# Performance work log

Measured on AMD Instinct MI355X. Metric: run time of the kernel, lower is better.

Reference implementation:

```python
import jax, jax.numpy as jnp
import numpy as np

B, S, D, H = 4, 2048, 1024, 16
HD = D // H  # head dim = 64


def setup_inputs() -> dict:
    key = jax.random.key(0)
    ks = jax.random.split(key, 11)
    sc = 1.0 / np.sqrt(D)
    return {
        "q": jax.random.normal(ks[0], (B, S, D), jnp.float32),
        "k": jax.random.normal(ks[1], (B, S, D), jnp.float32),
        "v": jax.random.normal(ks[2], (B, S, D), jnp.float32),
        "w_q": jax.random.normal(ks[3], (D, D), jnp.float32) * sc,
        "b_q": jnp.zeros((D,), jnp.float32),
        "w_k": jax.random.normal(ks[4], (D, D), jnp.float32) * sc,
        "b_k": jnp.zeros((D,), jnp.float32),
        "w_v": jax.random.normal(ks[5], (D, D), jnp.float32) * sc,
        "b_v": jnp.zeros((D,), jnp.float32),
        "w_fc": jax.random.normal(ks[6], (D, D), jnp.float32) * sc,
        "b_fc": jnp.zeros((D,), jnp.float32),
    }


def reference(q, k, v, w_q, b_q, w_k, b_k, w_v, b_v, w_fc, b_fc):
    scale = jnp.asarray(np.sqrt(HD), q.dtype)
    # QKV projections: [B,S,D] @ [D,D]^T (torch Linear: x @ W^T + b)
    Q = (q @ w_q.T + b_q).reshape(B, S, H, HD).transpose(0, 2, 1, 3)  # [B,H,S,HD]
    K = (k @ w_k.T + b_k).reshape(B, S, H, HD).transpose(0, 2, 1, 3)
    V = (v @ w_v.T + b_v).reshape(B, S, H, HD).transpose(0, 2, 1, 3)
    energy = jnp.einsum('bhqd,bhkd->bhqk', Q, K) / scale  # [B,H,S,S]
    attn = jax.nn.softmax(energy, axis=-1)  # dropout is identity in eval / p=0
    x = jnp.einsum('bhqk,bhkd->bhqd', attn, V)  # [B,H,S,HD]
    x = x.transpose(0, 2, 1, 3).reshape(B, S, D)
    return x @ w_fc.T + b_fc
```

## Files before the change

kernel.cpp:

```cpp
#include <hip/hip_runtime.h>
#include <stdint.h>

#define BN 4
#define SEQ 2048
#define DM 1024
#define NH 16
#define HD 64
#define ROWS (BN*SEQ)

typedef float  f32x4  __attribute__((ext_vector_type(4)));
typedef __bf16 bf16x8 __attribute__((ext_vector_type(8)));
typedef __bf16 bf16x4 __attribute__((ext_vector_type(4)));

#define QSCALE 0.18033688f

__device__ inline bf16x8 cvt8(const float* __restrict__ src) {
    float4 x0 = *(const float4*)src;
    float4 x1 = *(const float4*)(src + 4);
    bf16x8 r;
    r[0] = (__bf16)x0.x; r[1] = (__bf16)x0.y; r[2] = (__bf16)x0.z; r[3] = (__bf16)x0.w;
    r[4] = (__bf16)x1.x; r[5] = (__bf16)x1.y; r[6] = (__bf16)x1.z; r[7] = (__bf16)x1.w;
    return r;
}

__device__ inline void gl_lds16(const void* g, void* l) {
    __builtin_amdgcn_global_load_lds((const __attribute__((address_space(1))) uint32_t*)g,
                                     (__attribute__((address_space(3))) uint32_t*)l, 16, 0, 0);
}

__global__ __launch_bounds__(256) void cast3(
    const float* __restrict__ a0, const float* __restrict__ a1, const float* __restrict__ a2,
    __bf16* __restrict__ o0, __bf16* __restrict__ o1, __bf16* __restrict__ o2, int n8) {
    int t = blockIdx.x * 256 + threadIdx.x;
    if (t >= n8) return;
    const float* in = (blockIdx.y == 0) ? a0 : (blockIdx.y == 1) ? a1 : a2;
    __bf16* out     = (blockIdx.y == 0) ? o0 : (blockIdx.y == 1) ? o1 : o2;
    *(bf16x8*)&out[(size_t)t * 8] = cvt8(&in[(size_t)t * 8]);
}

__global__ __launch_bounds__(256) void cast4(
    const float* __restrict__ a0, const float* __restrict__ a1,
    const float* __restrict__ a2, const float* __restrict__ a3,
    __bf16* __restrict__ o0, __bf16* __restrict__ o1,
    __bf16* __restrict__ o2, __bf16* __restrict__ o3, int n8) {
    int t = blockIdx.x * 256 + threadIdx.x;
    if (t >= n8) return;
    const float* in = (blockIdx.y == 0) ? a0 : (blockIdx.y == 1) ? a1 : (blockIdx.y == 2) ? a2 : a3;
    __bf16* out     = (blockIdx.y == 0) ? o0 : (blockIdx.y == 1) ? o1 : (blockIdx.y == 2) ? o2 : o3;
    *(bf16x8*)&out[(size_t)t * 8] = cvt8(&in[(size_t)t * 8]);
}

#define GEMM_CORE_GLDS(Xp, Wp)                                                     \
    __shared__ __align__(16) __bf16 As[128 * 32];                                  \
    __shared__ __align__(16) __bf16 Bs[128 * 32];                                  \
    const int tid  = threadIdx.x;                                                  \
    const int lane = tid & 63;                                                     \
    const int wave = tid >> 6;                                                     \
    const int wm = (wave >> 1) * 64;                                               \
    const int wn = (wave & 1) * 64;                                                \
    const int c16 = lane & 15;                                                     \
    const int g8  = (lane >> 4) * 8;                                               \
    const int row0 = blockIdx.x * 128;                                             \
    const int col0 = blockIdx.y * 128;                                             \
    f32x4 acc[4][4] = {};                                                          \
    for (int k0 = 0; k0 < DM; k0 += 32) {                                          \
        __syncthreads();                                                           \
        _Pragma("unroll")                                                          \
        for (int h = 0; h < 2; h++) {                                              \
            int cidx = h * 256 + tid;                                              \
            gl_lds16(&Xp[(size_t)(row0 + (cidx >> 2)) * DM + k0 + (cidx & 3) * 8], \
                     &As[(size_t)(h * 256 + wave * 64) * 8]);                      \
            gl_lds16(&Wp[(size_t)(col0 + (cidx >> 2)) * DM + k0 + (cidx & 3) * 8], \
                     &Bs[(size_t)(h * 256 + wave * 64) * 8]);                      \
        }                                                                          \
        __syncthreads();                                                           \
        bf16x8 a[4], bfr[4];                                                       \
        _Pragma("unroll")                                                          \
        for (int i = 0; i < 4; i++) a[i]   = *(const bf16x8*)&As[(wm + i * 16 + c16) * 32 + g8]; \
        _Pragma("unroll")                                                          \
        for (int i = 0; i < 4; i++) bfr[i] = *(const bf16x8*)&Bs[(wn + i * 16 + c16) * 32 + g8]; \
        _Pragma("unroll")                                                          \
        for (int mi = 0; mi < 4; mi++)                                             \
            _Pragma("unroll")                                                      \
            for (int ni = 0; ni < 4; ni++)                                         \
                acc[mi][ni] = __builtin_amdgcn_mfma_f32_16x16x32_bf16(a[mi], bfr[ni], acc[mi][ni], 0, 0, 0); \
    }

__global__ __launch_bounds__(256) void gemm_qkv_f(
    const __bf16* __restrict__ qb, const __bf16* __restrict__ kb,
    const __bf16* __restrict__ vb,
    const __bf16* __restrict__ wqb, const __bf16* __restrict__ wkb,
    const __bf16* __restrict__ wvb,
    const float* __restrict__ bq, const float* __restrict__ bk,
    const float* __restrict__ bv,
    __bf16* __restrict__ Qp, __bf16* __restrict__ Kp, __bf16* __restrict__ Vt)
{
    const int z = blockIdx.z;
    const __bf16* X = (z == 0) ? qb : (z == 1) ? kb : vb;
    const __bf16* W = (z == 0) ? wqb : (z == 1) ? wkb : wvb;
    const float* bias = (z == 0) ? bq : (z == 1) ? bk : bv;

    GEMM_CORE_GLDS(X, W)

    if (z < 2) {
        __bf16* O = z ? Kp : Qp;
        const float qsc = z ? 1.0f : QSCALE;
        #pragma unroll
        for (int mi = 0; mi < 4; mi++) {
            int r0 = row0 + wm + mi * 16 + (lane >> 4) * 4;
            #pragma unroll
            for (int ni = 0; ni < 4; ni++) {
                int col = col0 + wn + ni * 16 + c16;
                float bsv = bias[col];
                int h = col >> 6, d = col & 63;
                #pragma unroll
                for (int i = 0; i < 4; i++) {
                    int r = r0 + i; int b = r >> 11, s = r & 2047;
                    O[((size_t)(b * NH + h) * SEQ + s) * HD + d] = (__bf16)((acc[mi][ni][i] + bsv) * qsc);
                }
            }
        }
    } else {
        #pragma unroll
        for (int mi = 0; mi < 4; mi++) {
            int r0 = row0 + wm + mi * 16 + (lane >> 4) * 4;
            #pragma unroll
            for (int ni = 0; ni < 4; ni++) {
                int col = col0 + wn + ni * 16 + c16;
                float bsv = bias[col];
                int h = col >> 6, d = col & 63;
                int b = r0 >> 11, s0 = r0 & 2047;
                size_t base = ((size_t)((b * NH + h) * HD + d)) * SEQ + s0;
                #pragma unroll
                for (int i = 0; i < 4; i++)
                    Vt[base + i] = (__bf16)(acc[mi][ni][i] + bsv);
            }
        }
    }
}

__global__ __launch_bounds__(256) void gemm_fc_f(
    const __bf16* __restrict__ Xc, const __bf16* __restrict__ Wfb,
    const float* __restrict__ bias, float* __restrict__ out)
{
    __shared__ __align__(16) __bf16 As[128 * 32];
    __shared__ __align__(16) __bf16 Bs[64 * 32];

    const int tid  = threadIdx.x;
    const int lane = tid & 63;
    const int wave = tid >> 6;
    const int wm = (wave >> 1) * 64;
    const int wn = (wave & 1) * 32;
    const int c16 = lane & 15;
    const int g8  = (lane >> 4) * 8;
    const int row0 = blockIdx.x * 128;
    const int col0 = blockIdx.y * 64;

    f32x4 acc[4][2] = {};
    for (int k0 = 0; k0 < DM; k0 += 32) {
        __syncthreads();
        #pragma unroll
        for (int h = 0; h < 2; h++) {
            int cidx = h * 256 + tid;
            gl_lds16(&Xc[(size_t)(row0 + (cidx >> 2)) * DM + k0 + (cidx & 3) * 8],
                     &As[(size_t)(h * 256 + wave * 64) * 8]);
        }
        gl_lds16(&Wfb[(size_t)(col0 + (tid >> 2)) * DM + k0 + (tid & 3) * 8],
                 &Bs[(size_t)(wave * 64) * 8]);
        __syncthreads();

        bf16x8 a[4], bfr[2];
        #pragma unroll
        for (int i = 0; i < 4; i++) a[i]   = *(const bf16x8*)&As[(wm + i * 16 + c16) * 32 + g8];
        #pragma unroll
        for (int i = 0; i < 2; i++) bfr[i] = *(const bf16x8*)&Bs[(wn + i * 16 + c16) * 32 + g8];
        #pragma unroll
        for (int mi = 0; mi < 4; mi++)
            #pragma unroll
            for (int ni = 0; ni < 2; ni++)
                acc[mi][ni] = __builtin_amdgcn_mfma_f32_16x16x32_bf16(a[mi], bfr[ni], acc[mi][ni], 0, 0, 0);
    }

    #pragma unroll
    for (int mi = 0; mi < 4; mi++) {
        int r0 = row0 + wm + mi * 16 + (lane >> 4) * 4;
        #pragma unroll
        for (int ni = 0; ni < 2; ni++) {
            int col = col0 + wn + ni * 16 + c16;
            float bsv = bias[col];
            #pragma unroll
            for (int i = 0; i < 4; i++)
                out[(size_t)(r0 + i) * DM + col] = acc[mi][ni][i] + bsv;
        }
    }
}

__global__ __launch_bounds__(256) void gemm_qk(
    const __bf16* __restrict__ qb, const __bf16* __restrict__ kb,
    const float* __restrict__ wqf, const float* __restrict__ wkf,
    const float* __restrict__ bq, const float* __restrict__ bk,
    __bf16* __restrict__ Qp, __bf16* __restrict__ Kp)
{
    const int z = blockIdx.z;
    const __bf16* X = z ? kb : qb;
    const float* W  = z ? wkf : wqf;
    const float* bias = z ? bk : bq;
    __bf16* O = z ? Kp : Qp;
    const float qsc = z ? 1.0f : QSCALE;

    __shared__ __align__(16) __bf16 As[128 * 32];
    __shared__ __align__(16) __bf16 Bs[128 * 32];

    const int tid  = threadIdx.x;
    const int lane = tid & 63;
    const int wave = tid >> 6;
    const int wm = (wave >> 1) * 64;
    const int wn = (wave & 1) * 64;
    const int c16 = lane & 15;
    const int g8  = (lane >> 4) * 8;
    const int row0 = blockIdx.x * 128;
    const int col0 = blockIdx.y * 128;
    const int brow = tid >> 1;
    const int bcc  = (tid & 1) * 16;

    f32x4 acc[4][4] = {};
    for (int k0 = 0; k0 < DM; k0 += 32) {
        __syncthreads();
        #pragma unroll
        for (int h = 0; h < 2; h++) {
            int cidx = h * 256 + tid;
            gl_lds16(&X[(size_t)(row0 + (cidx >> 2)) * DM + k0 + (cidx & 3) * 8],
                     &As[(size_t)(h * 256 + wave * 64) * 8]);
        }
        *(bf16x8*)&Bs[brow * 32 + bcc]     = cvt8(&W[(size_t)(col0 + brow) * DM + k0 + bcc]);
        *(bf16x8*)&Bs[brow * 32 + bcc + 8] = cvt8(&W[(size_t)(col0 + brow) * DM + k0 + bcc + 8]);
        __syncthreads();

        bf16x8 a[4], bfr[4];
        #pragma unroll
        for (int i = 0; i < 4; i++) a[i]   = *(const bf16x8*)&As[(wm + i * 16 + c16) * 32 + g8];
        #pragma unroll
        for (int i = 0; i < 4; i++) bfr[i] = *(const bf16x8*)&Bs[(wn + i * 16 + c16) * 32 + g8];
        #pragma unroll
        for (int mi = 0; mi < 4; mi++)
            #pragma unroll
            for (int ni = 0; ni < 4; ni++)
                acc[mi][ni] = __builtin_amdgcn_mfma_f32_16x16x32_bf16(a[mi], bfr[ni], acc[mi][ni], 0, 0, 0);
    }

    #pragma unroll
    for (int mi = 0; mi < 4; mi++) {
        int r0 = row0 + wm + mi * 16 + (lane >> 4) * 4;
        #pragma unroll
        for (int ni = 0; ni < 4; ni++) {
            int col = col0 + wn + ni * 16 + c16;
            float bsv = bias[col];
            int h = col >> 6, d = col & 63;
            #pragma unroll
            for (int i = 0; i < 4; i++) {
                int r = r0 + i; int b = r >> 11, s = r & 2047;
                O[((size_t)(b * NH + h) * SEQ + s) * HD + d] = (__bf16)((acc[mi][ni][i] + bsv) * qsc);
            }
        }
    }
}

__global__ __launch_bounds__(256) void gemm_v(
    const float* __restrict__ vf, const float* __restrict__ wvf,
    const float* __restrict__ bv, __bf16* __restrict__ Vt)
{
    __shared__ __align__(16) __bf16 As[128 * 32];
    __shared__ __align__(16) __bf16 Bs[128 * 32];

    const int tid  = threadIdx.x;
    const int lane = tid & 63;
    const int wave = tid >> 6;
    const int wm = (wave >> 1) * 64;
    const int wn = (wave & 1) * 64;
    const int c16 = lane & 15;
    const int g8  = (lane >> 4) * 8;
    const int row0 = blockIdx.x * 128;
    const int col0 = blockIdx.y * 128;
    const int brow = tid >> 1;
    const int bcc  = (tid & 1) * 16;

    f32x4 acc[4][4] = {};
    for (int k0 = 0; k0 < DM; k0 += 32) {
        __syncthreads();
        *(bf16x8*)&As[brow * 32 + bcc]     = cvt8(&vf[(size_t)(row0 + brow) * DM + k0 + bcc]);
        *(bf16x8*)&As[brow * 32 + bcc + 8] = cvt8(&vf[(size_t)(row0 + brow) * DM + k0 + bcc + 8]);
        *(bf16x8*)&Bs[brow * 32 + bcc]     = cvt8(&wvf[(size_t)(col0 + brow) * DM + k0 + bcc]);
        *(bf16x8*)&Bs[brow * 32 + bcc + 8] = cvt8(&wvf[(size_t)(col0 + brow) * DM + k0 + bcc + 8]);
        __syncthreads();

        bf16x8 a[4], bfr[4];
        #pragma unroll
        for (int i = 0; i < 4; i++) a[i]   = *(const bf16x8*)&As[(wm + i * 16 + c16) * 32 + g8];
        #pragma unroll
        for (int i = 0; i < 4; i++) bfr[i] = *(const bf16x8*)&Bs[(wn + i * 16 + c16) * 32 + g8];
        #pragma unroll
        for (int mi = 0; mi < 4; mi++)
            #pragma unroll
            for (int ni = 0; ni < 4; ni++)
                acc[mi][ni] = __builtin_amdgcn_mfma_f32_16x16x32_bf16(a[mi], bfr[ni], acc[mi][ni], 0, 0, 0);
    }

    #pragma unroll
    for (int mi = 0; mi < 4; mi++) {
        int r0 = row0 + wm + mi * 16 + (lane >> 4) * 4;
        #pragma unroll
        for (int ni = 0; ni < 4; ni++) {
            int col = col0 + wn + ni * 16 + c16;
            float bsv = bv[col];
            int h = col >> 6, d = col & 63;
            int b = r0 >> 11, s0 = r0 & 2047;
            size_t base = ((size_t)((b * NH + h) * HD + d)) * SEQ + s0;
            #pragma unroll
            for (int i = 0; i < 4; i++)
                Vt[base + i] = (__bf16)(acc[mi][ni][i] + bsv);
        }
    }
}

__global__ __launch_bounds__(256) void gemm_fc(
    const __bf16* __restrict__ Xc, const float* __restrict__ Wf,
    const float* __restrict__ bias, float* __restrict__ out)
{
    __shared__ __align__(16) __bf16 As[128 * 32];
    __shared__ __align__(16) __bf16 Bs[128 * 32];

    const int tid  = threadIdx.x;
    const int lane = tid & 63;
    const int wave = tid >> 6;
    const int wm = (wave >> 1) * 64;
    const int wn = (wave & 1) * 64;
    const int c16 = lane & 15;
    const int g8  = (lane >> 4) * 8;
    const int row0 = blockIdx.x * 128;
    const int col0 = blockIdx.y * 128;
    const int brow = tid >> 1;
    const int bcc  = (tid & 1) * 16;

    f32x4 acc[4][4] = {};
    for (int k0 = 0; k0 < DM; k0 += 32) {
        __syncthreads();
        #pragma unroll
        for (int h = 0; h < 2; h++) {
            int cidx = h * 256 + tid;
            gl_lds16(&Xc[(size_t)(row0 + (cidx >> 2)) * DM + k0 + (cidx & 3) * 8],
                     &As[(size_t)(h * 256 + wave * 64) * 8]);
        }
        *(bf16x8*)&Bs[brow * 32 + bcc]     = cvt8(&Wf[(size_t)(col0 + brow) * DM + k0 + bcc]);
        *(bf16x8*)&Bs[brow * 32 + bcc + 8] = cvt8(&Wf[(size_t)(col0 + brow) * DM + k0 + bcc + 8]);
        __syncthreads();

        bf16x8 a[4], bfr[4];
        #pragma unroll
        for (int i = 0; i < 4; i++) a[i]   = *(const bf16x8*)&As[(wm + i * 16 + c16) * 32 + g8];
        #pragma unroll
        for (int i = 0; i < 4; i++) bfr[i] = *(const bf16x8*)&Bs[(wn + i * 16 + c16) * 32 + g8];
        #pragma unroll
        for (int mi = 0; mi < 4; mi++)
            #pragma unroll
            for (int ni = 0; ni < 4; ni++)
                acc[mi][ni] = __builtin_amdgcn_mfma_f32_16x16x32_bf16(a[mi], bfr[ni], acc[mi][ni], 0, 0, 0);
    }

    #pragma unroll
    for (int mi = 0; mi < 4; mi++) {
        int r0 = row0 + wm + mi * 16 + (lane >> 4) * 4;
        #pragma unroll
        for (int ni = 0; ni < 4; ni++) {
            int col = col0 + wn + ni * 16 + c16;
            float bsv = bias[col];
            #pragma unroll
            for (int i = 0; i < 4; i++)
                out[(size_t)(r0 + i) * DM + col] = acc[mi][ni][i] + bsv;
        }
    }
}

__global__ __launch_bounds__(256, 4) void attn_kernel(
    const __bf16* __restrict__ Qp, const __bf16* __restrict__ Kp,
    const __bf16* __restrict__ Vt, __bf16* __restrict__ ctx)
{
    __shared__ __align__(16) __bf16 Ks[64 * 64];
    __shared__ __align__(16) __bf16 Vs[64 * 64];

    const int tid  = threadIdx.x;
    const int lane = tid & 63;
    const int w    = tid >> 6;
    const int bh   = blockIdx.x;
    const int q0   = blockIdx.y * 128 + w * 32;

    const __bf16* Qb = Qp + (size_t)bh * SEQ * HD;
    const __bf16* Kb = Kp + (size_t)bh * SEQ * HD;
    const __bf16* Vb = Vt + (size_t)bh * HD * SEQ;

    const int c16 = lane & 15;
    const int g   = lane >> 4;
    const int sw  = c16 & 7;

    bf16x8 qf[2][2];
    #pragma unroll
    for (int qs = 0; qs < 2; qs++)
        #pragma unroll
        for (int kc = 0; kc < 2; kc++)
            qf[qs][kc] = *(const bf16x8*)&Qb[(size_t)(q0 + qs * 16 + c16) * HD + kc * 32 + g * 8];

    float lp[2] = {0.f, 0.f};
    f32x4 o[4][2] = {};

    const int srow = (w * 16) + (lane >> 3);
    const int sj   = (lane & 7) ^ (lane >> 3);

    for (int kt = 0; kt < SEQ / 64; kt++) {
        const int k0 = kt * 64;
        __syncthreads();
        #pragma unroll
        for (int h = 0; h < 2; h++) {
            int r = srow + h * 8;
            gl_lds16(&Kb[(size_t)(k0 + r) * HD + sj * 8], &Ks[(size_t)(w * 16 + h * 8) * 64]);
            gl_lds16(&Vb[(size_t)r * SEQ + k0 + sj * 8],  &Vs[(size_t)(w * 16 + h * 8) * 64]);
        }
        __syncthreads();

        f32x4 sc[4][2] = {};
        __builtin_amdgcn_s_setprio(1);
        #pragma unroll
        for (int t = 0; t < 4; t++) {
            #pragma unroll
            for (int kc = 0; kc < 2; kc++) {
                bf16x8 kf = *(const bf16x8*)&Ks[(t * 16 + c16) * 64 + ((kc * 4 + g) ^ sw) * 8];
                sc[t][0] = __builtin_amdgcn_mfma_f32_16x16x32_bf16(kf, qf[0][kc], sc[t][0], 0, 0, 0);
                sc[t][1] = __builtin_amdgcn_mfma_f32_16x16x32_bf16(kf, qf[1][kc], sc[t][1], 0, 0, 0);
            }
        }
        __builtin_amdgcn_s_setprio(0);

        bf16x8 pf[2][2];
        #pragma unroll
        for (int qs = 0; qs < 2; qs++) {
            float ps = 0.f;
            #pragma unroll
            for (int kc = 0; kc < 2; kc++) {
                bf16x8 pv8;
                #pragma unroll
                for (int i = 0; i < 4; i++) {
                    float pv = exp2f(sc[2 * kc][qs][i]);
                    ps += pv; pv8[i] = (__bf16)pv;
                }
                #pragma unroll
                for (int i = 0; i < 4; i++) {
                    float pv = exp2f(sc[2 * kc + 1][qs][i]);
                    ps += pv; pv8[4 + i] = (__bf16)pv;
                }
                pf[qs][kc] = pv8;
            }
            lp[qs] += ps;
        }

        __builtin_amdgcn_s_setprio(1);
        #pragma unroll
        for (int t = 0; t < 4; t++) {
            #pragma unroll
            for (int kc = 0; kc < 2; kc++) {
                union { bf16x8 v8; bf16x4 v4[2]; } u;
                u.v4[0] = *(const bf16x4*)&Vs[(t * 16 + c16) * 64 + (((kc * 4 + (g >> 1)) ^ sw) * 8) + (g & 1) * 4];
                u.v4[1] = *(const bf16x4*)&Vs[(t * 16 + c16) * 64 + (((kc * 4 + 2 + (g >> 1)) ^ sw) * 8) + (g & 1) * 4];
                o[t][0] = __builtin_amdgcn_mfma_f32_16x16x32_bf16(u.v8, pf[0][kc], o[t][0], 0, 0, 0);
                o[t][1] = __builtin_amdgcn_mfma_f32_16x16x32_bf16(u.v8, pf[1][kc], o[t][1], 0, 0, 0);
            }
        }
        __builtin_amdgcn_s_setprio(0);
    }

    const int hh = bh & (NH - 1);
    const int bb = bh >> 4;
    #pragma unroll
    for (int qs = 0; qs < 2; qs++) {
        float l = lp[qs];
        l += __shfl_xor(l, 16, 64);
        l += __shfl_xor(l, 32, 64);
        float inv = 1.f / l;
        int s = q0 + qs * 16 + c16;
        #pragma unroll
        for (int t = 0; t < 4; t++) {
            bf16x4 ov;
            #pragma unroll
            for (int i = 0; i < 4; i++) ov[i] = (__bf16)(o[t][qs][i] * inv);
            *(bf16x4*)&ctx[((size_t)(bb * SEQ + s)) * DM + hh * HD + t * 16 + g * 4] = ov;
        }
    }
}

extern "C" void kernel_launch(void* const* d_in, const int* in_sizes, int n_in,
                              void* d_out, int out_size, void* d_ws, size_t ws_size,
                              hipStream_t stream) {
    const float* q    = (const float*)d_in[0];
    const float* k    = (const float*)d_in[1];
    const float* v    = (const float*)d_in[2];
    const float* w_q  = (const float*)d_in[3];
    const float* b_q  = (const float*)d_in[4];
    const float* w_k  = (const float*)d_in[5];
    const float* b_k  = (const float*)d_in[6];
    const float* w_v  = (const float*)d_in[7];
    const float* b_v  = (const float*)d_in[8];
    const float* w_fc = (const float*)d_in[9];
    const float* b_fc = (const float*)d_in[10];
    float* out = (float*)d_out;

    __bf16* qb = (__bf16*)d_out;
    __bf16* kb = qb + (size_t)ROWS * DM;

    char* p = (char*)d_ws;
    auto alloc = [&](size_t bytes) { char* r = p; p += (bytes + 255) & ~(size_t)255; return r; };
    const size_t XSZ = (size_t)ROWS * DM * 2;
    const size_t WSZ = (size_t)DM * DM * 2;

    __bf16* Qp  = (__bf16*)alloc(XSZ);
    __bf16* Kp  = (__bf16*)alloc(XSZ);
    __bf16* Vt  = (__bf16*)alloc(XSZ);
    __bf16* ctx = (__bf16*)alloc(XSZ);

    const size_t base_need = (size_t)(p - (char*)d_ws);
    const size_t fast_need = base_need + 4 * (WSZ + 256);

    const int n8x = ROWS * DM / 8;
    const int n8w = DM * DM / 8;

    __bf16* vb = ctx;

    cast3<<<dim3(n8x / 256, 3), 256, 0, stream>>>(q, k, v, qb, kb, vb, n8x);

    if (ws_size >= fast_need) {
        __bf16* wqb  = (__bf16*)alloc(WSZ);
        __bf16* wkb  = (__bf16*)alloc(WSZ);
        __bf16* wvb  = (__bf16*)alloc(WSZ);
        __bf16* wfcb = (__bf16*)alloc(WSZ);

        cast4<<<dim3(n8w / 256, 4), 256, 0, stream>>>(
            w_q, w_k, w_v, w_fc, wqb, wkb, wvb, wfcb, n8w);

        gemm_qkv_f<<<dim3(ROWS / 128, DM / 128, 3), 256, 0, stream>>>(
            qb, kb, vb, wqb, wkb, wvb, b_q, b_k, b_v, Qp, Kp, Vt);

        attn_kernel<<<dim3(BN * NH, SEQ / 128), 256, 0, stream>>>(Qp, Kp, Vt, ctx);

        gemm_fc_f<<<dim3(ROWS / 128, DM / 64), 256, 0, stream>>>(ctx, wfcb, b_fc, out);
    } else {
        gemm_v<<<dim3(ROWS / 128, DM / 128), 256, 0, stream>>>(v, w_v, b_v, Vt);
        gemm_qk<<<dim3(ROWS / 128, DM / 128, 2), 256, 0, stream>>>(
            qb, kb, w_q, w_k, b_q, b_k, Qp, Kp);

        attn_kernel<<<dim3(BN * NH, SEQ / 128), 256, 0, stream>>>(Qp, Kp, Vt, ctx);

        gemm_fc<<<dim3(ROWS / 128, DM / 128), 256, 0, stream>>>(ctx, w_fc, b_fc, out);
    }
}
```

Before: 367.4 us.

## Double-buffer K/V tiles in LDS and prefetch the next tile during compute

The attention kernel now keeps two LDS buffers each for K and V. It issues the global-to-LDS loads for tile kt+1 right after the barrier, then computes on tile kt, so one barrier per iteration replaces two and load latency can overlap with the MFMA and exp work. The s_setprio hints around the MFMA sections are also removed. The cost is double the LDS per block (32KB), which could limit occupancy. It also relies on the barrier's implicit memory wait to make the async LDS loads visible before use.

```diff
diff --git a/kernel.cpp b/kernel.cpp
--- a/kernel.cpp
+++ b/kernel.cpp
@@ -384,8 +384,8 @@
     const __bf16* __restrict__ Qp, const __bf16* __restrict__ Kp,
     const __bf16* __restrict__ Vt, __bf16* __restrict__ ctx)
 {
-    __shared__ __align__(16) __bf16 Ks[64 * 64];
-    __shared__ __align__(16) __bf16 Vs[64 * 64];
+    __shared__ __align__(16) __bf16 Ks[2][64 * 64];
+    __shared__ __align__(16) __bf16 Vs[2][64 * 64];
 
     const int tid  = threadIdx.x;
     const int lane = tid & 63;
@@ -414,29 +414,37 @@
     const int srow = (w * 16) + (lane >> 3);
     const int sj   = (lane & 7) ^ (lane >> 3);
 
-    for (int kt = 0; kt < SEQ / 64; kt++) {
+    auto stage = [&](int kt, int buf) {
         const int k0 = kt * 64;
-        __syncthreads();
         #pragma unroll
         for (int h = 0; h < 2; h++) {
             int r = srow + h * 8;
-            gl_lds16(&Kb[(size_t)(k0 + r) * HD + sj * 8], &Ks[(size_t)(w * 16 + h * 8) * 64]);
-            gl_lds16(&Vb[(size_t)r * SEQ + k0 + sj * 8],  &Vs[(size_t)(w * 16 + h * 8) * 64]);
-        }
-        __syncthreads();
+            gl_lds16(&Kb[(size_t)(k0 + r) * HD + sj * 8], &Ks[buf][(size_t)(w * 16 + h * 8) * 64]);
+            gl_lds16(&Vb[(size_t)r * SEQ + k0 + sj * 8],  &Vs[buf][(size_t)(w * 16 + h * 8) * 64]);
+        }
+    };
+
+    const int NT = SEQ / 64;
+    stage(0, 0);
+    int cur = 0;
+
+    for (int kt = 0; kt < NT; kt++) {
+        __syncthreads();
+        if (kt + 1 < NT) stage(kt + 1, cur ^ 1);
+
+        const __bf16* ksb = &Ks[cur][0];
+        const __bf16* vsb = &Vs[cur][0];
 
         f32x4 sc[4][2] = {};
-        __builtin_amdgcn_s_setprio(1);
         #pragma unroll
         for (int t = 0; t < 4; t++) {
             #pragma unroll
             for (int kc = 0; kc < 2; kc++) {
-                bf16x8 kf = *(const bf16x8*)&Ks[(t * 16 + c16) * 64 + ((kc * 4 + g) ^ sw) * 8];
+                bf16x8 kf = *(const bf16x8*)&ksb[(t * 16 + c16) * 64 + ((kc * 4 + g) ^ sw) * 8];
                 sc[t][0] = __builtin_amdgcn_mfma_f32_16x16x32_bf16(kf, qf[0][kc], sc[t][0], 0, 0, 0);
                 sc[t][1] = __builtin_amdgcn_mfma_f32_16x16x32_bf16(kf, qf[1][kc], sc[t][1], 0, 0, 0);
             }
         }
-        __builtin_amdgcn_s_setprio(0);
 
         bf16x8 pf[2][2];
         #pragma unroll
@@ -460,19 +468,19 @@
             lp[qs] += ps;
         }
 
-        __builtin_amdgcn_s_setprio(1);
         #pragma unroll
         for (int t = 0; t < 4; t++) {
             #pragma unroll
             for (int kc = 0; kc < 2; kc++) {
                 union { bf16x8 v8; bf16x4 v4[2]; } u;
-                u.v4[0] = *(const bf16x4*)&Vs[(t * 16 + c16) * 64 + (((kc * 4 + (g >> 1)) ^ sw) * 8) + (g & 1) * 4];
-                u.v4[1] = *(const bf16x4*)&Vs[(t * 16 + c16) * 64 + (((kc * 4 + 2 + (g >> 1)) ^ sw) * 8) + (g & 1) * 4];
+                u.v4[0] = *(const bf16x4*)&vsb[(t * 16 + c16) * 64 + (((kc * 4 + (g >> 1)) ^ sw) * 8) + (g & 1) * 4];
+                u.v4[1] = *(const bf16x4*)&vsb[(t * 16 + c16) * 64 + (((kc * 4 + 2 + (g >> 1)) ^ sw) * 8) + (g & 1) * 4];
                 o[t][0] = __builtin_amdgcn_mfma_f32_16x16x32_bf16(u.v8, pf[0][kc], o[t][0], 0, 0, 0);
                 o[t][1] = __builtin_amdgcn_mfma_f32_16x16x32_bf16(u.v8, pf[1][kc], o[t][1], 0, 0, 0);
             }
         }
-        __builtin_amdgcn_s_setprio(0);
+
+        cur ^= 1;
     }
 
     const int hh = bh & (NH - 1);
```

After: 360.2 us. Within noise of the previous version (-2.0%).

## Split attention over key range into two halves and combine with weighted merge

Applied to the files above, without the earlier changes.

Adds a split-KV variant of the attention kernel: each block handles half of the key sequence, writes normalized partial context plus row sums, and a separate combine kernel merges the halves by their softmax-denominator weights. Doubling the grid is meant to improve occupancy and load balance (the original grid is 1024 blocks). It adds an extra kernel launch and extra bf16 traffic for partial outputs, plus a bf16 rounding step before the merge. The macro refactor also drops the s_setprio hints from the shared attention body, which affects the unsplit path as well.

```diff
diff --git a/kernel.cpp b/kernel.cpp
--- a/kernel.cpp
+++ b/kernel.cpp
@@ -7,6 +7,7 @@
 #define NH 16
 #define HD 64
 #define ROWS (BN*SEQ)
+#define LSZ (BN*NH*SEQ)
 
 typedef float  f32x4  __attribute__((ext_vector_type(4)));
 typedef __bf16 bf16x8 __attribute__((ext_vector_type(8)));
@@ -380,100 +381,89 @@
     }
 }
 
+#define ATTN_BODY(KTLO, KTHI)                                                        \
+    __shared__ __align__(16) __bf16 Ks[64 * 64];                                     \
+    __shared__ __align__(16) __bf16 Vs[64 * 64];                                     \
+    const int tid  = threadIdx.x;                                                    \
+    const int lane = tid & 63;                                                       \
+    const int w    = tid >> 6;                                                       \
+    const int bh   = blockIdx.x;                                                     \
+    const int q0   = blockIdx.y * 128 + w * 32;                                      \
+    const __bf16* Qb = Qp + (size_t)bh * SEQ * HD;                                   \
+    const __bf16* Kb = Kp + (size_t)bh * SEQ * HD;                                   \
+    const __bf16* Vb = Vt + (size_t)bh * HD * SEQ;                                   \
+    const int c16 = lane & 15;                                                       \
+    const int g   = lane >> 4;                                                       \
+    const int sw  = c16 & 7;                                                         \
+    bf16x8 qf[2][2];                                                                 \
+    _Pragma("unroll")                                                                \
+    for (int qs = 0; qs < 2; qs++)                                                   \
+        _Pragma("unroll")                                                            \
+        for (int kc = 0; kc < 2; kc++)                                               \
+            qf[qs][kc] = *(const bf16x8*)&Qb[(size_t)(q0 + qs * 16 + c16) * HD + kc * 32 + g * 8]; \
+    float lp[2] = {0.f, 0.f};                                                        \
+    f32x4 o[4][2] = {};                                                              \
+    const int srow = (w * 16) + (lane >> 3);                                         \
+    const int sj   = (lane & 7) ^ (lane >> 3);                                       \
+    for (int kt = (KTLO); kt < (KTHI); kt++) {                                       \
+        const int k0 = kt * 64;                                                      \
+        __syncthreads();                                                             \
+        _Pragma("unroll")                                                            \
+        for (int h = 0; h < 2; h++) {                                                \
+            int r = srow + h * 8;                                                    \
+            gl_lds16(&Kb[(size_t)(k0 + r) * HD + sj * 8], &Ks[(size_t)(w * 16 + h * 8) * 64]); \
+            gl_lds16(&Vb[(size_t)r * SEQ + k0 + sj * 8],  &Vs[(size_t)(w * 16 + h * 8) * 64]); \
+        }                                                                            \
+        __syncthreads();                                                             \
+        f32x4 sc[4][2] = {};                                                         \
+        _Pragma("unroll")                                                            \
+        for (int t = 0; t < 4; t++) {                                                \
+            _Pragma("unroll")                                                        \
+            for (int kc = 0; kc < 2; kc++) {                                         \
+                bf16x8 kf = *(const bf16x8*)&Ks[(t * 16 + c16) * 64 + ((kc * 4 + g) ^ sw) * 8]; \
+                sc[t][0] = __builtin_amdgcn_mfma_f32_16x16x32_bf16(kf, qf[0][kc], sc[t][0], 0, 0, 0); \
+                sc[t][1] = __builtin_amdgcn_mfma_f32_16x16x32_bf16(kf, qf[1][kc], sc[t][1], 0, 0, 0); \
+            }                                                                        \
+        }                                                                            \
+        bf16x8 pf[2][2];                                                             \
+        _Pragma("unroll")                                                            \
+        for (int qs = 0; qs < 2; qs++) {                                             \
+            float ps = 0.f;                                                          \
+            _Pragma("unroll")                                                        \
+            for (int kc = 0; kc < 2; kc++) {                                         \
+                bf16x8 pv8;                                                          \
+                _Pragma("unroll")                                                    \
+                for (int i = 0; i < 4; i++) {                                        \
+                    float pv = exp2f(sc[2 * kc][qs][i]);                             \
+                    ps += pv; pv8[i] = (__bf16)pv;                                   \
+                }                                                                    \
+                _Pragma("unroll")                                                    \
+                for (int i = 0; i < 4; i++) {                                        \
+                    float pv = exp2f(sc[2 * kc + 1][qs][i]);                         \
+                    ps += pv; pv8[4 + i] = (__bf16)pv;                               \
+                }                                                                    \
+                pf[qs][kc] = pv8;                                                    \
+            }                                                                        \
+            lp[qs] += ps;                                                            \
+        }                                                                            \
+        _Pragma("unroll")                                                            \
+        for (int t = 0; t < 4; t++) {                                                \
+            _Pragma("unroll")                                                        \
+            for (int kc = 0; kc < 2; kc++) {                                         \
+                union { bf16x8 v8; bf16x4 v4[2]; } u;                                \
+                u.v4[0] = *(const bf16x4*)&Vs[(t * 16 + c16) * 64 + (((kc * 4 + (g >> 1)) ^ sw) * 8) + (g & 1) * 4]; \
+                u.v4[1] = *(const bf16x4*)&Vs[(t * 16 + c16) * 64 + (((kc * 4 + 2 + (g >> 1)) ^ sw) * 8) + (g & 1) * 4]; \
+                o[t][0] = __builtin_amdgcn_mfma_f32_16x16x32_bf16(u.v8, pf[0][kc], o[t][0], 0, 0, 0); \
+                o[t][1] = __builtin_amdgcn_mfma_f32_16x16x32_bf16(u.v8, pf[1][kc], o[t][1], 0, 0, 0); \
+            }                                                                        \
+        }                                                                            \
+    }
+
 __global__ __launch_bounds__(256, 4) void attn_kernel(
     const __bf16* __restrict__ Qp, const __bf16* __restrict__ Kp,
     const __bf16* __restrict__ Vt, __bf16* __restrict__ ctx)
 {
-    __shared__ __align__(16) __bf16 Ks[64 * 64];
-    __shared__ __align__(16) __bf16 Vs[64 * 64];
-
-    const int tid  = threadIdx.x;
-    const int lane = tid & 63;
-    const int w    = tid >> 6;
-    const int bh   = blockIdx.x;
-    const int q0   = blockIdx.y * 128 + w * 32;
-
-    const __bf16* Qb = Qp + (size_t)bh * SEQ * HD;
-    const __bf16* Kb = Kp + (size_t)bh * SEQ * HD;
-    const __bf16* Vb = Vt + (size_t)bh * HD * SEQ;
-
-    const int c16 = lane & 15;
-    const int g   = lane >> 4;
-    const int sw  = c16 & 7;
-
-    bf16x8 qf[2][2];
-    #pragma unroll
-    for (int qs = 0; qs < 2; qs++)
-        #pragma unroll
-        for (int kc = 0; kc < 2; kc++)
-            qf[qs][kc] = *(const bf16x8*)&Qb[(size_t)(q0 + qs * 16 + c16) * HD + kc * 32 + g * 8];
-
-    float lp[2] = {0.f, 0.f};
-    f32x4 o[4][2] = {};
-
-    const int srow = (w * 16) + (lane >> 3);
-    const int sj   = (lane & 7) ^ (lane >> 3);
-
-    for (int kt = 0; kt < SEQ / 64; kt++) {
-        const int k0 = kt * 64;
-        __syncthreads();
-        #pragma unroll
-        for (int h = 0; h < 2; h++) {
-            int r = srow + h * 8;
-            gl_lds16(&Kb[(size_t)(k0 + r) * HD + sj * 8], &Ks[(size_t)(w * 16 + h * 8) * 64]);
-            gl_lds16(&Vb[(size_t)r * SEQ + k0 + sj * 8],  &Vs[(size_t)(w * 16 + h * 8) * 64]);
-        }
-        __syncthreads();
-
-        f32x4 sc[4][2] = {};
-        __builtin_amdgcn_s_setprio(1);
-        #pragma unroll
-        for (int t = 0; t < 4; t++) {
-            #pragma unroll
-            for (int kc = 0; kc < 2; kc++) {
-                bf16x8 kf = *(const bf16x8*)&Ks[(t * 16 + c16) * 64 + ((kc * 4 + g) ^ sw) * 8];
-                sc[t][0] = __builtin_amdgcn_mfma_f32_16x16x32_bf16(kf, qf[0][kc], sc[t][0], 0, 0, 0);
-                sc[t][1] = __builtin_amdgcn_mfma_f32_16x16x32_bf16(kf, qf[1][kc], sc[t][1], 0, 0, 0);
-            }
-        }
-        __builtin_amdgcn_s_setprio(0);
-
-        bf16x8 pf[2][2];
-        #pragma unroll
-        for (int qs = 0; qs < 2; qs++) {
-            float ps = 0.f;
-            #pragma unroll
-            for (int kc = 0; kc < 2; kc++) {
-                bf16x8 pv8;
-                #pragma unroll
-                for (int i = 0; i < 4; i++) {
-                    float pv = exp2f(sc[2 * kc][qs][i]);
-                    ps += pv; pv8[i] = (__bf16)pv;
-                }
-                #pragma unroll
-                for (int i = 0; i < 4; i++) {
-                    float pv = exp2f(sc[2 * kc + 1][qs][i]);
-                    ps += pv; pv8[4 + i] = (__bf16)pv;
-                }
-                pf[qs][kc] = pv8;
-            }
-            lp[qs] += ps;
-        }
-
-        __builtin_amdgcn_s_setprio(1);
-        #pragma unroll
-        for (int t = 0; t < 4; t++) {
-            #pragma unroll
-            for (int kc = 0; kc < 2; kc++) {
-                union { bf16x8 v8; bf16x4 v4[2]; } u;
-                u.v4[0] = *(const bf16x4*)&Vs[(t * 16 + c16) * 64 + (((kc * 4 + (g >> 1)) ^ sw) * 8) + (g & 1) * 4];
-                u.v4[1] = *(const bf16x4*)&Vs[(t * 16 + c16) * 64 + (((kc * 4 + 2 + (g >> 1)) ^ sw) * 8) + (g & 1) * 4];
-                o[t][0] = __builtin_amdgcn_mfma_f32_16x16x32_bf16(u.v8, pf[0][kc], o[t][0], 0, 0, 0);
-                o[t][1] = __builtin_amdgcn_mfma_f32_16x16x32_bf16(u.v8, pf[1][kc], o[t][1], 0, 0, 0);
-            }
-        }
-        __builtin_amdgcn_s_setprio(0);
-    }
+    ATTN_BODY(0, SEQ / 64)
 
     const int hh = bh & (NH - 1);
     const int bb = bh >> 4;
@@ -492,6 +482,62 @@
             *(bf16x4*)&ctx[((size_t)(bb * SEQ + s)) * DM + hh * HD + t * 16 + g * 4] = ov;
         }
     }
+}
+
+__global__ __launch_bounds__(256, 4) void attn_split(
+    const __bf16* __restrict__ Qp, const __bf16* __restrict__ Kp,
+    const __bf16* __restrict__ Vt, __bf16* __restrict__ c0,
+    __bf16* __restrict__ c1, float* __restrict__ lsum)
+{
+    const int z = blockIdx.z;
+    const int ktlo = z * (SEQ / 128);
+
+    ATTN_BODY(ktlo, ktlo + SEQ / 128)
+
+    __bf16* co = z ? c1 : c0;
+    float*  ls = lsum + (size_t)z * LSZ;
+    const int hh = bh & (NH - 1);
+    const int bb = bh >> 4;
+    #pragma unroll
+    for (int qs = 0; qs < 2; qs++) {
+        float l = lp[qs];
+        l += __shfl_xor(l, 16, 64);
+        l += __shfl_xor(l, 32, 64);
+        float inv = 1.f / l;
+        int s = q0 + qs * 16 + c16;
+        if (g == 0) ls[(size_t)bh * SEQ + s] = l;
+        #pragma unroll
+        for (int t = 0; t < 4; t++) {
+            bf16x4 ov;
+            #pragma unroll
+            for (int i = 0; i < 4; i++) ov[i] = (__bf16)(o[t][qs][i] * inv);
+            *(bf16x4*)&co[((size_t)(bb * SEQ + s)) * DM + hh * HD + t * 16 + g * 4] = ov;
+        }
+    }
+}
+
+__global__ __launch_bounds__(256) void attn_combine(
+    __bf16* __restrict__ c0, const __bf16* __restrict__ c1,
+    const float* __restrict__ lsum)
+{
+    int t = blockIdx.x * 256 + threadIdx.x;
+    size_t r = (size_t)t * 8;
+    int bs  = t >> 7;
+    int dmo = (t & 127) * 8;
+    int hh = dmo >> 6;
+    int bb = bs >> 11, s = bs & 2047;
+    int bh = bb * NH + hh;
+    float l0 = lsum[(size_t)bh * SEQ + s];
+    float l1 = lsum[(size_t)LSZ + (size_t)bh * SEQ + s];
+    float inv = 1.f / (l0 + l1);
+    float w0 = l0 * inv, w1 = l1 * inv;
+    bf16x8 a = *(const bf16x8*)&c0[r];
+    bf16x8 b = *(const bf16x8*)&c1[r];
+    bf16x8 ov;
+    #pragma unroll
+    for (int i = 0; i < 8; i++)
+        ov[i] = (__bf16)(w0 * (float)a[i] + w1 * (float)b[i]);
+    *(bf16x8*)&c0[r] = ov;
 }
 
 extern "C" void kernel_launch(void* const* d_in, const int* in_sizes, int n_in,
@@ -524,7 +570,8 @@
     __bf16* ctx = (__bf16*)alloc(XSZ);
 
     const size_t base_need = (size_t)(p - (char*)d_ws);
-    const size_t fast_need = base_need + 4 * (WSZ + 256);
+    const size_t fast_need  = base_need + 4 * (WSZ + 256);
+    const size_t split_need = fast_need + (XSZ + 256) + (2 * LSZ * 4 + 256);
 
     const int n8x = ROWS * DM / 8;
     const int n8w = DM * DM / 8;
@@ -545,7 +592,15 @@
         gemm_qkv_f<<<dim3(ROWS / 128, DM / 128, 3), 256, 0, stream>>>(
             qb, kb, vb, wqb, wkb, wvb, b_q, b_k, b_v, Qp, Kp, Vt);
 
-        attn_kernel<<<dim3(BN * NH, SEQ / 128), 256, 0, stream>>>(Qp, Kp, Vt, ctx);
+        if (ws_size >= split_need) {
+            __bf16* ctx1 = (__bf16*)alloc(XSZ);
+            float*  lsum = (float*)alloc(2 * LSZ * 4);
+            attn_split<<<dim3(BN * NH, SEQ / 128, 2), 256, 0, stream>>>(
+                Qp, Kp, Vt, ctx, ctx1, lsum);
+            attn_combine<<<n8x / 256, 256, 0, stream>>>(ctx, ctx1, lsum);
+        } else {
+            attn_kernel<<<dim3(BN * NH, SEQ / 128), 256, 0, stream>>>(Qp, Kp, Vt, ctx);
+        }
 
         gemm_fc_f<<<dim3(ROWS / 128, DM / 64), 256, 0, stream>>>(ctx, wfcb, b_fc, out);
     } else {
```

Measured after the change: 366.2 us. No clear change (-0.3%).
